# Optimization experiments

Measured on AMD Instinct MI355X. Metric: run time of the kernel, lower is better.

## Reference

```python
import jax, jax.numpy as jnp
import numpy as np

B, T, E, H = 8, 2048, 1024, 128

def setup_inputs() -> dict:
    key = jax.random.key(0)
    kx, kq, kk, kv = jax.random.split(key, 4)
    x = jax.random.normal(kx, (B, T, E), dtype=jnp.float32)
    # Linear(E, H, bias=False) weights, stored as (E, H) so y = x @ W
    s = 1.0 / np.sqrt(E)
    Wq = jax.random.normal(kq, (E, H), dtype=jnp.float32) * s
    Wk = jax.random.normal(kk, (E, H), dtype=jnp.float32) * s
    Wv = jax.random.normal(kv, (E, H), dtype=jnp.float32) * s
    return {"x": x, "Wq": Wq, "Wk": Wk, "Wv": Wv}

def reference(x, Wq, Wk, Wv):
    # x: (B, T, E)
    Tcur = x.shape[1]
    q = jnp.einsum('bte,eh->bth', x, Wq)
    k = jnp.einsum('bte,eh->bth', x, Wk)
    v = jnp.einsum('bte,eh->bth', x, Wv)
    scores = jnp.einsum('bqh,bkh->bqk', q, k)  # (B, T, T)
    # NOTE: source multiplies by x.shape[2]**0.5 where x.shape[2] == T here
    scores = scores * jnp.sqrt(jnp.asarray(Tcur, dtype=scores.dtype))
    causal = jnp.tril(jnp.ones((Tcur, Tcur), dtype=bool))
    scores = jnp.where(causal, scores, -jnp.inf)
    attn = jax.nn.softmax(scores, axis=2)
    # dropout p=0.0 -> identity
    return jnp.einsum('bqk,bkh->bqh', attn, v)
```

## Files before the change

### kernel.cpp

```cpp
#include <hip/hip_runtime.h>
#include <hip/hip_bf16.h>
#include <math.h>

#define B_ 8
#define T_ 2048
#define E_ 1024
#define H_ 128
#define M_ (B_*T_)
#define SCALE_ 45.25483399593904f
#define SEG_ 4

typedef __attribute__((ext_vector_type(8))) short bf16x8;
typedef __attribute__((ext_vector_type(4))) float f32x4;

#define mfma16(A, Bv, C) __builtin_amdgcn_mfma_f32_16x16x32_bf16((A), (Bv), (C), 0, 0, 0)

#define FRAGW(g, kc, lane)  ((((size_t)(g)*32 + (kc))*64 + (lane))*8)
#define FRAGK(b, kt16, kc, lane) (((((size_t)(b)*128 + (kt16))*4 + (kc))*64 + (lane))*8)
#define FRAGV(b, ht, kt32, lane) (((((size_t)(b)*8 + (ht))*64 + (kt32))*64 + (lane))*8)

__device__ __forceinline__ ushort bf16_rne(float f) {
  unsigned u = __float_as_uint(f);
  u += 0x7fffu + ((u >> 16) & 1u);
  return (ushort)(u >> 16);
}
__device__ __forceinline__ float bf16_tof(ushort h) {
  return __uint_as_float(((unsigned)h) << 16);
}

__device__ __forceinline__ void lds_barrier() {
  asm volatile("s_waitcnt lgkmcnt(0)" ::: "memory");
  __builtin_amdgcn_s_barrier();
}

__global__ __launch_bounds__(256) void wsplit(
    const float* __restrict__ Wq, const float* __restrict__ Wk,
    const float* __restrict__ Wv,
    ushort* __restrict__ whT, ushort* __restrict__ wlT)
{
  const int idx  = blockIdx.x * 256 + threadIdx.x;
  const int mat  = idx >> 14;
  const int rem  = idx & 16383;
  const int nt   = rem >> 11;
  const int kc   = (rem >> 6) & 31;
  const int lane = rem & 63;
  const int quad = lane >> 4, l15 = lane & 15;
  const float* W = (mat == 0) ? Wq : (mat == 1) ? Wk : Wv;
  const int n  = nt * 16 + l15;
  const int k0 = kc * 32 + quad * 8;
  bf16x8 hv, lv;
  #pragma unroll
  for (int j = 0; j < 8; ++j) {
    const float f = W[(size_t)(k0 + j) * H_ + n];
    const ushort h = bf16_rne(f);
    hv[j] = (short)h;
    lv[j] = (short)bf16_rne(f - bf16_tof(h));
  }
  *(bf16x8*)(whT + (size_t)idx * 8) = hv;
  *(bf16x8*)(wlT + (size_t)idx * 8) = lv;
}

#define CVT8W(F0, F1, DSTOFF) do {                                            \
    const float f_[8] = {(F0).x, (F0).y, (F0).z, (F0).w,                      \
                         (F1).x, (F1).y, (F1).z, (F1).w};                     \
    bf16x8 hv_, lv_;                                                          \
    _Pragma("unroll")                                                         \
    for (int jj_ = 0; jj_ < 8; ++jj_) {                                       \
      const ushort h_ = bf16_rne(f_[jj_]);                                    \
      hv_[jj_] = (short)h_;                                                   \
      lv_[jj_] = (short)bf16_rne(f_[jj_] - bf16_tof(h_));                     \
    }                                                                         \
    *(bf16x8*)&SM[(DSTOFF) + ca * 8] = hv_;                                   \
    *(bf16x8*)&SM[(DSTOFF) + 2048 + ca * 8] = lv_;                            \
  } while (0)

#define AFRAG(CUR, HALFOFF, MT) \
    (*(const bf16x8*)&SM[(CUR)*8192 + (HALFOFF) + \
        (((MT)*4 + quad)*16 + (l15 ^ quad))*8])

#define PSTEP4(S, CUR, NXT, BHC, BLC, BHN, BLN) do {                          \
    bf16x8 ah_[4], al_[4];                                                    \
    _Pragma("unroll")                                                         \
    for (int mt_ = 0; mt_ < 4; ++mt_) {                                       \
      ah_[mt_] = AFRAG(CUR, 0,    mt_);                                       \
      al_[mt_] = AFRAG(CUR, 2048, mt_);                                       \
    }                                                                         \
    if ((S) + 1 < 16) {                                                       \
      _Pragma("unroll")                                                       \
      for (int kch_ = 0; kch_ < 2; ++kch_) {                                  \
        const int kcn_ = 2*((S)+1) + kch_;                                    \
        BHN[kch_*3+0] = *(const bf16x8*)(whT + FRAGW(gq,     kcn_, lane));    \
        BHN[kch_*3+1] = *(const bf16x8*)(whT + FRAGW(gq + 4, kcn_, lane));    \
        BHN[kch_*3+2] = *(const bf16x8*)(whT + FRAGW(gv,     kcn_, lane));    \
        BLN[kch_*2+0] = *(const bf16x8*)(wlT + FRAGW(gq,     kcn_, lane));    \
        BLN[kch_*2+1] = *(const bf16x8*)(wlT + FRAGW(gq + 4, kcn_, lane));    \
      }                                                                       \
    }                                                                         \
    float4 nx0_, nx1_, nx2_, nx3_;                                            \
    if ((S) + 2 < 16) {                                                       \
      nx0_ = *(const float4*)(xrow + 64*((S)+2));                             \
      nx1_ = *(const float4*)(xrow + 64*((S)+2) + 4);                         \
      nx2_ = *(const float4*)(xrow + 64*((S)+2) + 32);                        \
      nx3_ = *(const float4*)(xrow + 64*((S)+2) + 36);                        \
    } else { nx0_ = xf0; nx1_ = xf1; nx2_ = xf2; nx3_ = xf3; }                \
    __builtin_amdgcn_s_setprio(1);                                            \
    _Pragma("unroll")                                                         \
    for (int mt_ = 0; mt_ < 4; ++mt_) {                                       \
      acc[0][mt_] = mfma16(ah_[mt_], BHC[0], acc[0][mt_]);                    \
      acc[0][mt_] = mfma16(ah_[mt_], BLC[0], acc[0][mt_]);                    \
      acc[0][mt_] = mfma16(al_[mt_], BHC[0], acc[0][mt_]);                    \
      acc[1][mt_] = mfma16(ah_[mt_], BHC[1], acc[1][mt_]);                    \
      acc[1][mt_] = mfma16(ah_[mt_], BLC[1], acc[1][mt_]);                    \
      acc[1][mt_] = mfma16(al_[mt_], BHC[1], acc[1][mt_]);                    \
      acc[2][mt_] = mfma16(ah_[mt_], BHC[2], acc[2][mt_]);                    \
    }                                                                         \
    __builtin_amdgcn_s_setprio(0);                                            \
    if ((S) + 1 < 16) {                                                       \
      CVT8W(xf0, xf1, (NXT)*8192);                                            \
      CVT8W(xf2, xf3, (NXT)*8192 + 4096);                                     \
    }                                                                         \
    _Pragma("unroll")                                                         \
    for (int mt_ = 0; mt_ < 4; ++mt_) {                                       \
      ah_[mt_] = AFRAG(CUR, 4096, mt_);                                       \
      al_[mt_] = AFRAG(CUR, 6144, mt_);                                       \
    }                                                                         \
    __builtin_amdgcn_s_setprio(1);                                            \
    _Pragma("unroll")                                                         \
    for (int mt_ = 0; mt_ < 4; ++mt_) {                                       \
      acc[0][mt_] = mfma16(ah_[mt_], BHC[3], acc[0][mt_]);                    \
      acc[0][mt_] = mfma16(ah_[mt_], BLC[2], acc[0][mt_]);                    \
      acc[0][mt_] = mfma16(al_[mt_], BHC[3], acc[0][mt_]);                    \
      acc[1][mt_] = mfma16(ah_[mt_], BHC[4], acc[1][mt_]);                    \
      acc[1][mt_] = mfma16(ah_[mt_], BLC[3], acc[1][mt_]);                    \
      acc[1][mt_] = mfma16(al_[mt_], BHC[4], acc[1][mt_]);                    \
      acc[2][mt_] = mfma16(ah_[mt_], BHC[5], acc[2][mt_]);                    \
    }                                                                         \
    __builtin_amdgcn_s_setprio(0);                                            \
    xf0 = nx0_; xf1 = nx1_; xf2 = nx2_; xf3 = nx3_;                           \
    lds_barrier();                                                            \
  } while (0)

__global__ __launch_bounds__(256, 2) void proj_fused(
    const float* __restrict__ x,
    const ushort* __restrict__ whT, const ushort* __restrict__ wlT,
    ushort* __restrict__ qh, ushort* __restrict__ ql,
    ushort* __restrict__ kfh, ushort* __restrict__ kfl,
    ushort* __restrict__ vF)
{
  const int m0   = blockIdx.x * 64;
  const int half = blockIdx.y;
  const int tid  = threadIdx.x;
  const int wave = tid >> 6, lane = tid & 63;
  const int quad = lane >> 4, l15 = lane & 15;

  __shared__ __align__(16) ushort SM[16384];

  f32x4 acc[3][4];
  #pragma unroll
  for (int j = 0; j < 3; ++j)
    #pragma unroll
    for (int mt = 0; mt < 4; ++mt) acc[j][mt] = (f32x4){0.f, 0.f, 0.f, 0.f};

  const int arow  = tid >> 2;
  const int akoff = (tid & 3) * 8;
  const int ca    = ((arow >> 4) * 4 + (tid & 3)) * 16
                    + ((arow & 15) ^ (tid & 3));
  const int gq    = half * 8 + wave;
  const int gv    = 16 + half * 4 + wave;

  const float* xrow = x + (size_t)(m0 + arow) * E_ + akoff;

  float4 xf0, xf1, xf2, xf3;
  bf16x8 bhA[6], blA[4], bhB[6], blB[4];

  {
    const float4 a0 = *(const float4*)(xrow);
    const float4 a1 = *(const float4*)(xrow + 4);
    const float4 a2 = *(const float4*)(xrow + 32);
    const float4 a3 = *(const float4*)(xrow + 36);
    CVT8W(a0, a1, 0);
    CVT8W(a2, a3, 4096);
    xf0 = *(const float4*)(xrow + 64);
    xf1 = *(const float4*)(xrow + 68);
    xf2 = *(const float4*)(xrow + 96);
    xf3 = *(const float4*)(xrow + 100);
    #pragma unroll
    for (int kch = 0; kch < 2; ++kch) {
      bhA[kch*3+0] = *(const bf16x8*)(whT + FRAGW(gq,     kch, lane));
      bhA[kch*3+1] = *(const bf16x8*)(whT + FRAGW(gq + 4, kch, lane));
      bhA[kch*3+2] = *(const bf16x8*)(whT + FRAGW(gv,     kch, lane));
      blA[kch*2+0] = *(const bf16x8*)(wlT + FRAGW(gq,     kch, lane));
      blA[kch*2+1] = *(const bf16x8*)(wlT + FRAGW(gq + 4, kch, lane));
    }
  }
  lds_barrier();

  int s = 0;
  while (true) {
    PSTEP4(s, 0, 1, bhA, blA, bhB, blB); if (++s == 16) break;
    PSTEP4(s, 1, 0, bhB, blB, bhA, blA); if (++s == 16) break;
  }

  {
    ushort* TB = SM;
    const int colbase = wave * 16 + l15;
    const int bb = m0 >> 11, t0 = m0 & 2047;
    #pragma unroll
    for (int pass = 0; pass < 2; ++pass) {
      __syncthreads();
      #pragma unroll
      for (int j = 0; j < 2; ++j)
        #pragma unroll
        for (int mt = 0; mt < 4; ++mt)
          #pragma unroll
          for (int r = 0; r < 4; ++r) {
            const float a = acc[j][mt][r];
            const ushort h = bf16_rne(a);
            const ushort val = pass ? bf16_rne(a - bf16_tof(h)) : h;
            TB[(mt * 16 + quad * 4 + r) * 136 + colbase + j * 64] = val;
          }
      __syncthreads();
      if (half == 0) {
        const int row = tid >> 2, c0 = (tid & 3) * 32;
        ushort* dst = (pass ? ql : qh) + (size_t)(m0 + row) * H_ + c0;
        #pragma unroll
        for (int u = 0; u < 4; ++u)
          *(bf16x8*)(dst + u * 8) = *(const bf16x8*)&TB[row * 136 + c0 + u * 8];
      } else {
        ushort* dstb = (pass ? kfl : kfh) + FRAGK(bb, t0 >> 4, 0, 0) + tid * 32;
        const int kt16l = tid >> 6;
        const int kcc   = (tid >> 4) & 3;
        const int lane0 = (tid & 15) * 4;
        #pragma unroll
        for (int u = 0; u < 4; ++u) {
          const int l  = lane0 + u;
          const int key = kt16l * 16 + (l & 15);
          const int h0  = kcc * 32 + (l >> 4) * 8;
          *(bf16x8*)(dstb + u * 8) = *(const bf16x8*)&TB[key * 136 + h0];
        }
      }
    }
  }
  __syncthreads();
  {
    ushort* smT = SM;
    const int lh = wave * 16 + l15;
    #pragma unroll
    for (int mt = 0; mt < 4; ++mt)
      #pragma unroll
      for (int r = 0; r < 4; ++r)
        smT[lh * 72 + mt * 16 + quad * 4 + r] = bf16_rne(acc[2][mt][r]);
    __syncthreads();
    const int bb = m0 >> 11, t0 = m0 & 2047;
    #pragma unroll
    for (int u = 0; u < 2; ++u) {
      const int c    = u * 256 + tid;
      const int lht  = c >> 7;
      const int ktl  = (c >> 6) & 1;
      const int lv   = c & 63;
      const int qv   = lv >> 4, l15v = lv & 15;
      *(bf16x8*)(vF + FRAGV(bb, half * 4 + lht, (t0 >> 5) + ktl, lv)) =
          *(const bf16x8*)&smT[(lht * 16 + l15v) * 72 + ktl * 32 + qv * 8];
    }
  }
}

__global__ __launch_bounds__(256) void attn_flash(
    const ushort* __restrict__ qh, const ushort* __restrict__ ql,
    const ushort* __restrict__ kfh, const ushort* __restrict__ kfl,
    const ushort* __restrict__ vF,
    ushort* __restrict__ Opart, float* __restrict__ mlpart)
{
  const int b    = (int)blockIdx.x & 7;
  const int seg  = (int)blockIdx.x >> 3;
  const int qt   = 31 - (int)blockIdx.y;
  const int q0   = qt * 64;
  const int tid  = threadIdx.x;
  const int wave = tid >> 6, lane = tid & 63;
  const int quad = lane >> 4, l15 = lane & 15;
  const f32x4 z4 = (f32x4){0.f, 0.f, 0.f, 0.f};

  __shared__ __align__(16) unsigned smPw[1280];
  __shared__ __align__(16) ushort  smO[8704];
  unsigned* pw = smPw + wave * 320;

  const int ntiles = 2 * qt + 2;
  const int cnt    = (ntiles + SEG_ - 1) >> 2;
  const int jt0    = seg * cnt;
  const int jt1    = (jt0 + cnt < ntiles) ? (jt0 + cnt) : ntiles;

  const int q0w = q0 + wave * 16;
  const int ntw = ((q0w + 15) >> 5) + 1;
  const size_t pidx = ((size_t)(b * 128 + qt * 4 + wave)) * SEG_ + seg;
  ushort* op = Opart + pidx * 2048;
  float*  ml = mlpart + pidx * 32;

  if (jt0 >= jt1) {
    const bf16x8 zz = {0, 0, 0, 0, 0, 0, 0, 0};
    #pragma unroll
    for (int u = 0; u < 4; ++u)
      *(bf16x8*)(op + lane * 32 + u * 8) = zz;
    if (lane < 32) ml[lane] = (lane & 1) ? 0.f : -1e30f;
    return;
  }

  const size_t base = (size_t)b * T_ * H_;

  const ushort* qhp = qh + base + (size_t)(q0w + l15) * H_ + quad * 8;
  const ushort* qlp = ql + base + (size_t)(q0w + l15) * H_ + quad * 8;
  bf16x8 Qh[4], Ql[4];
  #pragma unroll
  for (int c = 0; c < 4; ++c) {
    Qh[c] = *(const bf16x8*)(qhp + c * 32);
    Ql[c] = *(const bf16x8*)(qlp + c * 32);
  }

  f32x4 O[8];
  #pragma unroll
  for (int i = 0; i < 8; ++i) O[i] = z4;
  float mst = -1e30f;
  float lst = 0.f;

  const size_t kvb = (size_t)b * 262144;
  const int jtc = (jt1 < ntw) ? jt1 : ntw;

  for (int jt = jt0; jt < jtc; ++jt) {
    const ushort* pKh = kfh + kvb + (size_t)jt * 4096;
    const ushort* pKl = kfl + kvb + (size_t)jt * 4096;
    const ushort* pV  = vF  + kvb + (size_t)jt * 512;
    const int k0 = jt * 32;

    f32x4 shh0 = z4, shh1 = z4, sx0 = z4, sx1 = z4;
    #pragma unroll
    for (int c = 0; c < 4; ++c) {
      const bf16x8 kh0 = *(const bf16x8*)(pKh + c * 512 + lane * 8);
      const bf16x8 kh1 = *(const bf16x8*)(pKh + (4 + c) * 512 + lane * 8);
      const bf16x8 kl0 = *(const bf16x8*)(pKl + c * 512 + lane * 8);
      const bf16x8 kl1 = *(const bf16x8*)(pKl + (4 + c) * 512 + lane * 8);
      shh0 = mfma16(kh0, Qh[c], shh0);
      shh1 = mfma16(kh1, Qh[c], shh1);
      sx0  = mfma16(kl0, Qh[c], sx0);
      sx1  = mfma16(kl1, Qh[c], sx1);
      sx0  = mfma16(kh0, Ql[c], sx0);
      sx1  = mfma16(kh1, Ql[c], sx1);
    }

    float r0[4], r1[4];
    #pragma unroll
    for (int r = 0; r < 4; ++r) {
      r0[r] = shh0[r] + sx0[r];
      r1[r] = shh1[r] + sx1[r];
    }
    if (jt == ntw - 1) {
      const int base0 = q0w + l15 - k0 - quad * 4;
      #pragma unroll
      for (int r = 0; r < 4; ++r) {
        if (r > base0)      r0[r] = -1e30f;
        if (r > base0 - 16) r1[r] = -1e30f;
      }
    }

    float pm = fmaxf(fmaxf(fmaxf(r0[0], r0[1]), fmaxf(r0[2], r0[3])),
                     fmaxf(fmaxf(r1[0], r1[1]), fmaxf(r1[2], r1[3])));
    pm = fmaxf(pm, __shfl_xor(pm, 16));
    pm = fmaxf(pm, __shfl_xor(pm, 32));

    const float mnew  = fmaxf(mst, pm);
    const float alpha = __expf((mst - mnew) * SCALE_);
    mst = mnew;

    float p0[4], p1[4];
    #pragma unroll
    for (int r = 0; r < 4; ++r) {
      p0[r] = __expf((r0[r] - mnew) * SCALE_);
      p1[r] = __expf((r1[r] - mnew) * SCALE_);
    }
    float sm = ((p0[0] + p0[1]) + (p0[2] + p0[3])) +
               ((p1[0] + p1[1]) + (p1[2] + p1[3]));
    sm += __shfl_xor(sm, 16);
    sm += __shfl_xor(sm, 32);
    lst = lst * alpha + sm;

    const unsigned w0 = (unsigned)bf16_rne(p0[0]) | ((unsigned)bf16_rne(p0[1]) << 16);
    const unsigned w1 = (unsigned)bf16_rne(p0[2]) | ((unsigned)bf16_rne(p0[3]) << 16);
    const unsigned w2 = (unsigned)bf16_rne(p1[0]) | ((unsigned)bf16_rne(p1[1]) << 16);
    const unsigned w3 = (unsigned)bf16_rne(p1[2]) | ((unsigned)bf16_rne(p1[3]) << 16);
    *(unsigned long long*)&pw[l15 * 20 + 2 * quad] =
        (unsigned long long)w0 | ((unsigned long long)w1 << 32);
    *(unsigned long long*)&pw[l15 * 20 + 8 + 2 * quad] =
        (unsigned long long)w2 | ((unsigned long long)w3 << 32);

    #pragma unroll
    for (int ct = 0; ct < 8; ++ct) {
      O[ct][0] *= alpha; O[ct][1] *= alpha;
      O[ct][2] *= alpha; O[ct][3] *= alpha;
    }
    const bf16x8 pB = *(const bf16x8*)&pw[l15 * 20 + 4 * quad];
    #pragma unroll
    for (int ct = 0; ct < 8; ++ct) {
      const bf16x8 vf = *(const bf16x8*)(pV + ct * 32768 + lane * 8);
      O[ct] = mfma16(vf, pB, O[ct]);
    }
  }

  {
    ushort* so = smO + wave * 2176;
    #pragma unroll
    for (int ct = 0; ct < 8; ++ct)
      #pragma unroll
      for (int r = 0; r < 4; ++r)
        so[l15 * 136 + ct * 16 + quad * 4 + r] = bf16_rne(O[ct][r]);
    #pragma unroll
    for (int u = 0; u < 4; ++u) {
      const int q_ = u * 4 + quad;
      *(bf16x8*)(op + q_ * 128 + l15 * 8) =
          *(const bf16x8*)&so[q_ * 136 + l15 * 8];
    }
  }
  if (quad == 0) {
    ml[l15 * 2]     = mst * SCALE_;
    ml[l15 * 2 + 1] = lst;
  }
}

__global__ __launch_bounds__(256) void attn_combine(
    const ushort* __restrict__ Opart, const float* __restrict__ mlpart,
    float* __restrict__ out)
{
  const int idx = blockIdx.x * 256 + threadIdx.x;
  const int c4  = idx & 31;
  const int r   = idx >> 5;
  const int t   = r & 2047;
  const int qt  = t >> 4, r16 = t & 15;
  const size_t pb = ((size_t)((r >> 11) * 128 + qt)) * SEG_;

  float m[SEG_], l[SEG_];
  #pragma unroll
  for (int s = 0; s < SEG_; ++s) {
    m[s] = mlpart[(pb + s) * 32 + r16 * 2];
    l[s] = mlpart[(pb + s) * 32 + r16 * 2 + 1];
  }
  float M = m[0];
  #pragma unroll
  for (int s = 1; s < SEG_; ++s) M = fmaxf(M, m[s]);
  float w[SEG_], L = 0.f;
  #pragma unroll
  for (int s = 0; s < SEG_; ++s) {
    w[s] = __expf(m[s] - M);
    L += l[s] * w[s];
  }
  float4 acc = make_float4(0.f, 0.f, 0.f, 0.f);
  #pragma unroll
  for (int s = 0; s < SEG_; ++s) {
    const ushort4 o = *(const ushort4*)(Opart + (pb + s) * 2048 + r16 * 128 + c4 * 4);
    acc.x += w[s] * bf16_tof(o.x);
    acc.y += w[s] * bf16_tof(o.y);
    acc.z += w[s] * bf16_tof(o.z);
    acc.w += w[s] * bf16_tof(o.w);
  }
  const float inv = 1.0f / L;
  *(float4*)(out + (size_t)r * H_ + c4 * 4) =
      make_float4(acc.x * inv, acc.y * inv, acc.z * inv, acc.w * inv);
}

extern "C" void kernel_launch(void* const* d_in, const int* in_sizes, int n_in,
                              void* d_out, int out_size, void* d_ws, size_t ws_size,
                              hipStream_t stream) {
  (void)in_sizes; (void)n_in; (void)out_size; (void)ws_size;
  const float* x  = (const float*)d_in[0];
  const float* Wq = (const float*)d_in[1];
  const float* Wk = (const float*)d_in[2];
  const float* Wv = (const float*)d_in[3];
  float* out = (float*)d_out;

  ushort* qhb = (ushort*)d_ws;
  ushort* qlb = qhb + (size_t)M_ * H_;
  ushort* kfh = qlb + (size_t)M_ * H_;
  ushort* kfl = kfh + (size_t)M_ * H_;
  ushort* vFb = kfl + (size_t)M_ * H_;
  ushort* whT = vFb + (size_t)M_ * H_;
  ushort* wlT = whT + (size_t)3 * H_ * E_;
  ushort* Opart = wlT + (size_t)3 * H_ * E_;
  float*  mlpart = (float*)(Opart + (size_t)B_ * 128 * SEG_ * 2048);

  wsplit<<<dim3(192), 256, 0, stream>>>(Wq, Wk, Wv, whT, wlT);
  proj_fused<<<dim3(M_/64, 2), 256, 0, stream>>>(x, whT, wlT,
                                                 qhb, qlb, kfh, kfl, vFb);
  attn_flash<<<dim3(B_*SEG_, 32), 256, 0, stream>>>(qhb, qlb, kfh, kfl, vFb,
                                                    Opart, mlpart);
  attn_combine<<<dim3(2048), 256, 0, stream>>>(Opart, mlpart, out);
}
```

Baseline: 166.3 us.

## Double K-step depth in projection GEMM to halve barriers

```diff
diff --git a/kernel.cpp b/kernel.cpp
--- a/kernel.cpp
+++ b/kernel.cpp
@@ -74,69 +74,83 @@
     *(bf16x8*)&SM[(DSTOFF) + 2048 + ca * 8] = lv_;                            \
   } while (0)
 
-#define AFRAG(CUR, HALFOFF, MT) \
-    (*(const bf16x8*)&SM[(CUR)*8192 + (HALFOFF) + \
-        (((MT)*4 + quad)*16 + (l15 ^ quad))*8])
-
-#define PSTEP4(S, CUR, NXT, BHC, BLC, BHN, BLN) do {                          \
+#define APH(CUR, P, MT) (*(const bf16x8*)&SM[(CUR)*16384 + (P)*4096 + \
+    (((MT)*4 + quad)*16 + (l15 ^ quad))*8])
+#define ALH(CUR, P, MT) (*(const bf16x8*)&SM[(CUR)*16384 + (P)*4096 + 2048 + \
+    (((MT)*4 + quad)*16 + (l15 ^ quad))*8])
+
+#define MPHASE(CUR, P, BH0, BH1, BH2, BL0, BL1) do {                          \
     bf16x8 ah_[4], al_[4];                                                    \
     _Pragma("unroll")                                                         \
     for (int mt_ = 0; mt_ < 4; ++mt_) {                                       \
-      ah_[mt_] = AFRAG(CUR, 0,    mt_);                                       \
-      al_[mt_] = AFRAG(CUR, 2048, mt_);                                       \
-    }                                                                         \
-    if ((S) + 1 < 16) {                                                       \
-      _Pragma("unroll")                                                       \
-      for (int kch_ = 0; kch_ < 2; ++kch_) {                                  \
-        const int kcn_ = 2*((S)+1) + kch_;                                    \
-        BHN[kch_*3+0] = *(const bf16x8*)(whT + FRAGW(gq,     kcn_, lane));    \
-        BHN[kch_*3+1] = *(const bf16x8*)(whT + FRAGW(gq + 4, kcn_, lane));    \
-        BHN[kch_*3+2] = *(const bf16x8*)(whT + FRAGW(gv,     kcn_, lane));    \
-        BLN[kch_*2+0] = *(const bf16x8*)(wlT + FRAGW(gq,     kcn_, lane));    \
-        BLN[kch_*2+1] = *(const bf16x8*)(wlT + FRAGW(gq + 4, kcn_, lane));    \
-      }                                                                       \
-    }                                                                         \
-    float4 nx0_, nx1_, nx2_, nx3_;                                            \
-    if ((S) + 2 < 16) {                                                       \
-      nx0_ = *(const float4*)(xrow + 64*((S)+2));                             \
-      nx1_ = *(const float4*)(xrow + 64*((S)+2) + 4);                         \
-      nx2_ = *(const float4*)(xrow + 64*((S)+2) + 32);                        \
-      nx3_ = *(const float4*)(xrow + 64*((S)+2) + 36);                        \
-    } else { nx0_ = xf0; nx1_ = xf1; nx2_ = xf2; nx3_ = xf3; }                \
+      ah_[mt_] = APH(CUR, P, mt_);                                            \
+      al_[mt_] = ALH(CUR, P, mt_);                                            \
+    }                                                                         \
     __builtin_amdgcn_s_setprio(1);                                            \
     _Pragma("unroll")                                                         \
     for (int mt_ = 0; mt_ < 4; ++mt_) {                                       \
-      acc[0][mt_] = mfma16(ah_[mt_], BHC[0], acc[0][mt_]);                    \
-      acc[0][mt_] = mfma16(ah_[mt_], BLC[0], acc[0][mt_]);                    \
-      acc[0][mt_] = mfma16(al_[mt_], BHC[0], acc[0][mt_]);                    \
-      acc[1][mt_] = mfma16(ah_[mt_], BHC[1], acc[1][mt_]);                    \
-      acc[1][mt_] = mfma16(ah_[mt_], BLC[1], acc[1][mt_]);                    \
-      acc[1][mt_] = mfma16(al_[mt_], BHC[1], acc[1][mt_]);                    \
-      acc[2][mt_] = mfma16(ah_[mt_], BHC[2], acc[2][mt_]);                    \
+      acc[0][mt_] = mfma16(ah_[mt_], BH0, acc[0][mt_]);                       \
+      acc[0][mt_] = mfma16(ah_[mt_], BL0, acc[0][mt_]);                       \
+      acc[0][mt_] = mfma16(al_[mt_], BH0, acc[0][mt_]);                       \
+      acc[1][mt_] = mfma16(ah_[mt_], BH1, acc[1][mt_]);                       \
+      acc[1][mt_] = mfma16(ah_[mt_], BL1, acc[1][mt_]);                       \
+      acc[1][mt_] = mfma16(al_[mt_], BH1, acc[1][mt_]);                       \
+      acc[2][mt_] = mfma16(ah_[mt_], BH2, acc[2][mt_]);                       \
     }                                                                         \
     __builtin_amdgcn_s_setprio(0);                                            \
-    if ((S) + 1 < 16) {                                                       \
-      CVT8W(xf0, xf1, (NXT)*8192);                                            \
-      CVT8W(xf2, xf3, (NXT)*8192 + 4096);                                     \
-    }                                                                         \
+  } while (0)
+
+#define BLOADX(KCN0) do {                                                     \
     _Pragma("unroll")                                                         \
-    for (int mt_ = 0; mt_ < 4; ++mt_) {                                       \
-      ah_[mt_] = AFRAG(CUR, 4096, mt_);                                       \
-      al_[mt_] = AFRAG(CUR, 6144, mt_);                                       \
-    }                                                                         \
-    __builtin_amdgcn_s_setprio(1);                                            \
+    for (int kch_ = 0; kch_ < 2; ++kch_) {                                    \
+      const int kcn_ = (KCN0) + kch_;                                         \
+      bhX[kch_*3+0] = *(const bf16x8*)(whT + FRAGW(gq,     kcn_, lane));      \
+      bhX[kch_*3+1] = *(const bf16x8*)(whT + FRAGW(gq + 4, kcn_, lane));      \
+      bhX[kch_*3+2] = *(const bf16x8*)(whT + FRAGW(gv,     kcn_, lane));      \
+      blX[kch_*2+0] = *(const bf16x8*)(wlT + FRAGW(gq,     kcn_, lane));      \
+      blX[kch_*2+1] = *(const bf16x8*)(wlT + FRAGW(gq + 4, kcn_, lane));      \
+    }                                                                         \
+  } while (0)
+
+#define BLOADY(KCN0) do {                                                     \
     _Pragma("unroll")                                                         \
-    for (int mt_ = 0; mt_ < 4; ++mt_) {                                       \
-      acc[0][mt_] = mfma16(ah_[mt_], BHC[3], acc[0][mt_]);                    \
-      acc[0][mt_] = mfma16(ah_[mt_], BLC[2], acc[0][mt_]);                    \
-      acc[0][mt_] = mfma16(al_[mt_], BHC[3], acc[0][mt_]);                    \
-      acc[1][mt_] = mfma16(ah_[mt_], BHC[4], acc[1][mt_]);                    \
-      acc[1][mt_] = mfma16(ah_[mt_], BLC[3], acc[1][mt_]);                    \
-      acc[1][mt_] = mfma16(al_[mt_], BHC[4], acc[1][mt_]);                    \
-      acc[2][mt_] = mfma16(ah_[mt_], BHC[5], acc[2][mt_]);                    \
-    }                                                                         \
-    __builtin_amdgcn_s_setprio(0);                                            \
-    xf0 = nx0_; xf1 = nx1_; xf2 = nx2_; xf3 = nx3_;                           \
+    for (int kch_ = 0; kch_ < 2; ++kch_) {                                    \
+      const int kcn_ = (KCN0) + kch_;                                         \
+      bhY[kch_*3+0] = *(const bf16x8*)(whT + FRAGW(gq,     kcn_, lane));      \
+      bhY[kch_*3+1] = *(const bf16x8*)(whT + FRAGW(gq + 4, kcn_, lane));      \
+      bhY[kch_*3+2] = *(const bf16x8*)(whT + FRAGW(gv,     kcn_, lane));      \
+      blY[kch_*2+0] = *(const bf16x8*)(wlT + FRAGW(gq,     kcn_, lane));      \
+      blY[kch_*2+1] = *(const bf16x8*)(wlT + FRAGW(gq + 4, kcn_, lane));      \
+    }                                                                         \
+  } while (0)
+
+#define XLOAD(SOFF) do {                                                      \
+    xf0 = *(const float4*)(xrow + (SOFF));                                    \
+    xf1 = *(const float4*)(xrow + (SOFF) + 4);                                \
+    xf2 = *(const float4*)(xrow + (SOFF) + 32);                               \
+    xf3 = *(const float4*)(xrow + (SOFF) + 36);                               \
+    xf4 = *(const float4*)(xrow + (SOFF) + 64);                               \
+    xf5 = *(const float4*)(xrow + (SOFF) + 68);                               \
+    xf6 = *(const float4*)(xrow + (SOFF) + 96);                               \
+    xf7 = *(const float4*)(xrow + (SOFF) + 100);                              \
+  } while (0)
+
+#define PSTEP8(S, CUR, NXT) do {                                              \
+    MPHASE(CUR, 0, bhX[0], bhX[1], bhX[2], blX[0], blX[1]);                   \
+    MPHASE(CUR, 1, bhX[3], bhX[4], bhX[5], blX[2], blX[3]);                   \
+    if ((S) + 1 < 8) {                                                        \
+      BLOADX(4*((S)+1));                                                      \
+      CVT8W(xf0, xf1, (NXT)*16384);                                           \
+      CVT8W(xf2, xf3, (NXT)*16384 + 4096);                                    \
+    }                                                                         \
+    MPHASE(CUR, 2, bhY[0], bhY[1], bhY[2], blY[0], blY[1]);                   \
+    MPHASE(CUR, 3, bhY[3], bhY[4], bhY[5], blY[2], blY[3]);                   \
+    if ((S) + 1 < 8) {                                                        \
+      BLOADY(4*((S)+1) + 2);                                                  \
+      CVT8W(xf4, xf5, (NXT)*16384 + 8192);                                    \
+      CVT8W(xf6, xf7, (NXT)*16384 + 12288);                                   \
+    }                                                                         \
+    if ((S) + 2 < 8) XLOAD(128*((S)+2));                                      \
     lds_barrier();                                                            \
   } while (0)
 
@@ -153,7 +167,7 @@
   const int wave = tid >> 6, lane = tid & 63;
   const int quad = lane >> 4, l15 = lane & 15;
 
-  __shared__ __align__(16) ushort SM[16384];
+  __shared__ __align__(16) ushort SM[32768];
 
   f32x4 acc[3][4];
   #pragma unroll
@@ -170,35 +184,32 @@
 
   const float* xrow = x + (size_t)(m0 + arow) * E_ + akoff;
 
-  float4 xf0, xf1, xf2, xf3;
-  bf16x8 bhA[6], blA[4], bhB[6], blB[4];
+  float4 xf0, xf1, xf2, xf3, xf4, xf5, xf6, xf7;
+  bf16x8 bhX[6], blX[4], bhY[6], blY[4];
 
   {
     const float4 a0 = *(const float4*)(xrow);
     const float4 a1 = *(const float4*)(xrow + 4);
     const float4 a2 = *(const float4*)(xrow + 32);
     const float4 a3 = *(const float4*)(xrow + 36);
+    const float4 a4 = *(const float4*)(xrow + 64);
+    const float4 a5 = *(const float4*)(xrow + 68);
+    const float4 a6 = *(const float4*)(xrow + 96);
+    const float4 a7 = *(const float4*)(xrow + 100);
     CVT8W(a0, a1, 0);
     CVT8W(a2, a3, 4096);
-    xf0 = *(const float4*)(xrow + 64);
-    xf1 = *(const float4*)(xrow + 68);
-    xf2 = *(const float4*)(xrow + 96);
-    xf3 = *(const float4*)(xrow + 100);
-    #pragma unroll
-    for (int kch = 0; kch < 2; ++kch) {
-      bhA[kch*3+0] = *(const bf16x8*)(whT + FRAGW(gq,     kch, lane));
-      bhA[kch*3+1] = *(const bf16x8*)(whT + FRAGW(gq + 4, kch, lane));
-      bhA[kch*3+2] = *(const bf16x8*)(whT + FRAGW(gv,     kch, lane));
-      blA[kch*2+0] = *(const bf16x8*)(wlT + FRAGW(gq,     kch, lane));
-      blA[kch*2+1] = *(const bf16x8*)(wlT + FRAGW(gq + 4, kch, lane));
-    }
+    CVT8W(a4, a5, 8192);
+    CVT8W(a6, a7, 12288);
+    XLOAD(128);
+    BLOADX(0);
+    BLOADY(2);
   }
   lds_barrier();
 
   int s = 0;
   while (true) {
-    PSTEP4(s, 0, 1, bhA, blA, bhB, blB); if (++s == 16) break;
-    PSTEP4(s, 1, 0, bhB, blB, bhA, blA); if (++s == 16) break;
+    PSTEP8(s, 0, 1); if (++s == 8) break;
+    PSTEP8(s, 1, 0); if (++s == 8) break;
   }
 
   {
```

Result: no change. 165.5 us (-0.5%).
